# Performance work log

Hardware: AMD Instinct MI355X
Metric: run time of the kernel (lower is better)

The kernel has to match this reference:

```python
import jax, jax.numpy as jnp
import numpy as np

N = 524288
NUM_LEVELS = 16
FEATS = 2
LOG2_T = 19
TABLE = 1 << LOG2_T
MIN_RES, MAX_RES = 16, 1024
PRIMES = np.array([1, 2654435761, 805459861], dtype=np.uint32)
_growth = np.exp((np.log(MAX_RES) - np.log(MIN_RES)) / (NUM_LEVELS - 1))
SCALINGS = np.floor(MIN_RES * _growth ** np.arange(NUM_LEVELS)).astype(np.float32)  # [L]


def hash_encode(positions, table):
    # positions [N,3] in [0,1]; table [L*T, F]
    scaled = positions[:, None, :] * jnp.asarray(SCALINGS)[None, :, None]  # [N,L,3]
    fl = jnp.floor(scaled)
    ce = jnp.ceil(scaled)
    offset = scaled - fl  # [N,L,3]
    primes = jnp.asarray(PRIMES)  # [3] uint32
    lvl_off = jnp.arange(NUM_LEVELS, dtype=jnp.uint32) * jnp.uint32(TABLE)  # [L]
    out = jnp.zeros(scaled.shape[:2] + (FEATS,), scaled.dtype)
    for corner in range(8):
        bits = np.array([(corner >> d) & 1 for d in range(3)], dtype=np.float32)
        coord = jnp.where(jnp.asarray(bits, dtype=bool), ce, fl)
        h = coord.astype(jnp.int32).astype(jnp.uint32) * primes  # [N,L,3]
        h = h[..., 0] ^ h[..., 1] ^ h[..., 2]
        idx = ((h & jnp.uint32(TABLE - 1)) + lvl_off).astype(jnp.int32)  # [N,L]
        b = jnp.asarray(bits)
        w = jnp.prod(b * offset + (1.0 - b) * (1.0 - offset), axis=-1, keepdims=True)  # [N,L,1]
        out = out + w * table[idx]
    return out.reshape(out.shape[0], NUM_LEVELS * FEATS)  # [N,32]


def nerf_encode(d):
    # NeRFEncoding: 4 freqs in 2**linspace(0,4,4), include_input=True -> 27 dims
    freqs = 2.0 ** jnp.linspace(0.0, 4.0, 4)
    scaled = (2.0 * jnp.pi * d)[..., None] * freqs  # [N,3,4]
    scaled = scaled.reshape(d.shape[0], -1)  # [N,12]
    enc = jnp.sin(jnp.concatenate([scaled, scaled + jnp.pi / 2.0], axis=-1))  # [N,24]
    return jnp.concatenate([enc, d], axis=-1)  # [N,27]


def setup_inputs() -> dict:
    key = jax.random.key(0)
    ks = jax.random.split(key, 16)
    w = lambda k, i, o: jax.random.normal(k, (i, o), jnp.float32) * (1.0 / np.sqrt(i))
    return {
        "positions": jax.random.uniform(ks[0], (N, 3), jnp.float32),
        "directions": jax.random.normal(ks[1], (N, 3), jnp.float32),
        "hash_table": (jax.random.uniform(ks[2], (NUM_LEVELS * TABLE, FEATS), jnp.float32) * 2.0 - 1.0) * 1e-3,
        "w0": w(ks[3], 32, 64), "b0": jnp.zeros((64,), jnp.float32),
        "w1": w(ks[4], 64, 64), "b1": jnp.zeros((64,), jnp.float32),
        "w2": w(ks[5], 64, 64), "b2": jnp.zeros((64,), jnp.float32),
        "wr": w(ks[6], 91, 32), "br": jnp.zeros((32,), jnp.float32),
        "wc": w(ks[7], 32, 3), "bc": jnp.zeros((3,), jnp.float32),
        "wd": w(ks[8], 64, 1), "bd": jnp.zeros((1,), jnp.float32),
    }


def reference(positions, directions, hash_table, w0, b0, w1, b1, w2, b2, wr, br, wc, bc, wd, bd):
    enc_xyz = hash_encode(positions, hash_table)  # [N,32]
    enc_dir = nerf_encode(directions)  # [N,27]
    h = jax.nn.relu(enc_xyz @ w0 + b0)
    h = jax.nn.relu(h @ w1 + b1)
    base = h @ w2 + b2  # [N,64], linear out (out_activation=None)
    rgb_h = jnp.concatenate([enc_dir, base], axis=-1) @ wr + br  # [N,32], single layer
    rgb = jax.nn.sigmoid(rgb_h @ wc + bc)  # [N,3]
    density = jax.nn.softplus(base @ wd + bd)  # [N,1]
    return jnp.concatenate([rgb, density], axis=-1)  # [N,4]
```

## Files before the change

kernel.cpp:

```cpp
#include <hip/hip_runtime.h>
#include <math.h>

#define NPTS 524288
#define LOG2T 19
#define TSIZE (1u << LOG2T)
#define TMASK (TSIZE - 1u)

typedef unsigned int uint32;
typedef unsigned short ushort16;

typedef __attribute__((ext_vector_type(8))) short short8;
typedef __attribute__((ext_vector_type(4))) float f32x4;

__device__ __forceinline__ float bf2f(ushort16 u) {
    union { uint32 i; float f; } v; v.i = ((uint32)u) << 16; return v.f;
}
__device__ __forceinline__ ushort16 f2bf(float f) {
    union { float f; uint32 i; } v; v.f = f;
    uint32 r = v.i + 0x7fffu + ((v.i >> 16) & 1u);
    return (ushort16)(r >> 16);
}
__device__ __forceinline__ uint32 pack2(float a, float b) {
    uint32 r;
    asm("v_cvt_pk_bf16_f32 %0, %1, %2" : "=v"(r) : "v"(a), "v"(b));
    return r;
}
__device__ __forceinline__ float ldin(const void* p, int i, bool f32) {
    return f32 ? ((const float*)p)[i] : bf2f(((const ushort16*)p)[i]);
}

struct Scal16 { float s[16]; };
struct Freq4  { float f[4]; };
struct HashP  { float s[16]; int dD[8]; int doff[8]; };
struct DenseP { int dD[6]; int pfx[7]; };

__global__ __launch_bounds__(256) void k_prep(const void* __restrict__ pos,
                                              const void* __restrict__ tbl,
                                              uint4* __restrict__ tbl2F,
                                              uint4* __restrict__ dense4,
                                              DenseP dp) {
    __shared__ int sFlag;
    int tid = threadIdx.x;
    if (tid < 64) {
        const ushort16* ph = (const ushort16*)pos;
        float v0 = bf2f(ph[tid]), v1 = bf2f(ph[tid + 64]);
        bool odd = !(fabsf(v0) <= 4.f) || !(fabsf(v1) <= 4.f);
        unsigned long long m = __ballot(odd);
        if (tid == 0) sFlag = (m != 0ull) ? 1 : 0;
    }
    __syncthreads();
    const bool f32 = (sFlag != 0);

    if (blockIdx.x < 5120) {
        if (!f32) return;
        const float4* tf4 = (const float4*)tbl;
        size_t g = (size_t)blockIdx.x * 256 + tid;
        float4 v0 = tf4[(size_t)3 * TSIZE + 2 * g];
        float4 v1 = tf4[(size_t)3 * TSIZE + 2 * g + 1];
        uint4 o;
        o.x = pack2(v0.x, v0.y); o.y = pack2(v0.z, v0.w);
        o.z = pack2(v1.x, v1.y); o.w = pack2(v1.z, v1.w);
        tbl2F[g] = o;
        return;
    }

    int e = (blockIdx.x - 5120) * 256 + tid;
    if (e >= dp.pfx[6]) return;
    int l = 0;
#pragma unroll
    for (int k = 1; k < 6; ++k) l += (e >= dp.pfx[k]) ? 1 : 0;
    int c = e - dp.pfx[l];
    int D = dp.dD[l], D2 = D * D;
    int cz = c / D2; int rm = c - cz * D2;
    int cy = rm / D; int cx = rm - cy * D;

    uint32 base = (uint32)l << LOG2T;
    uint32 hz  = (uint32)cz * 805459861u;
    uint32 hy0 = (uint32)cy * 2654435761u;
    uint32 hy1 = (uint32)(cy + 1) * 2654435761u;
    uint32 h00 = ((((uint32)cx)       ^ hy0 ^ hz) & TMASK) + base;
    uint32 h10 = ((((uint32)(cx + 1)) ^ hy0 ^ hz) & TMASK) + base;
    uint32 h01 = ((((uint32)cx)       ^ hy1 ^ hz) & TMASK) + base;
    uint32 h11 = ((((uint32)(cx + 1)) ^ hy1 ^ hz) & TMASK) + base;

    uint4 o;
    if (f32) {
        const float2* t2 = (const float2*)tbl;
        float2 a = t2[h00], b = t2[h10], cc = t2[h01], d = t2[h11];
        o.x = pack2(a.x, a.y); o.y = pack2(b.x, b.y);
        o.z = pack2(cc.x, cc.y); o.w = pack2(d.x, d.y);
    } else {
        const uint32* t1 = (const uint32*)tbl;
        o.x = t1[h00]; o.y = t1[h10]; o.z = t1[h01]; o.w = t1[h11];
    }
    dense4[e] = o;
}

__global__ __launch_bounds__(256) void k_denseEnc(const void* __restrict__ pos,
                                                  const uint4* __restrict__ dense4,
                                                  uint32* __restrict__ enc,
                                                  HashP hp) {
    __shared__ __align__(16) uint4 sPosQ[192];
    __shared__ int sFlag;
    int tid = threadIdx.x;
    if (tid < 64) {
        const ushort16* ph = (const ushort16*)pos;
        float v0 = bf2f(ph[tid]), v1 = bf2f(ph[tid + 64]);
        bool odd = !(fabsf(v0) <= 4.f) || !(fabsf(v1) <= 4.f);
        unsigned long long m = __ballot(odd);
        if (tid == 0) sFlag = (m != 0ull) ? 1 : 0;
    }
    __syncthreads();
    const bool f32 = (sFlag != 0);

    int p0 = blockIdx.x * 256;
    int pt = p0 + tid;

    {
        int n16 = f32 ? 192 : 96;
        const uint4* src = (const uint4*)((const char*)pos + (size_t)p0 * (f32 ? 12 : 6));
        for (int i = tid; i < n16; i += 256) sPosQ[i] = src[i];
    }
    __syncthreads();

    float x, y, z;
    if (f32) {
        const float* pf = (const float*)sPosQ;
        x = pf[3 * tid]; y = pf[3 * tid + 1]; z = pf[3 * tid + 2];
    } else {
        const ushort16* ph2 = (const ushort16*)sPosQ;
        x = bf2f(ph2[3 * tid]); y = bf2f(ph2[3 * tid + 1]); z = bf2f(ph2[3 * tid + 2]);
    }

#pragma unroll
    for (int l = 0; l < 6; ++l) {
        float s = hp.s[l];
        float sx = x * s, sy = y * s, sz = z * s;
        float fx = floorf(sx), fy = floorf(sy), fz = floorf(sz);
        float cx = ceilf(sx), cy = ceilf(sy), cz = ceilf(sz);
        float ox = sx - fx, oy = sy - fy, oz = sz - fz;
        float wx0 = 1.f - ox, wy0 = 1.f - oy, wz0 = 1.f - oz;

        int D = hp.dD[l], D2 = D * D;
        int fxi = (int)fx, fyi = (int)fy, fzi = (int)fz;
        bool dxb = ((int)cx != fxi);
        bool dyb = ((int)cy != fyi);
        bool dzb = ((int)cz != fzi);
        const uint4* dp4 = dense4 + hp.doff[l];
        int i0 = fxi + fyi * D + fzi * D2;
        uint4 P0 = dp4[i0];
        uint4 P1 = dp4[i0 + (dzb ? D2 : 0)];

        float a0 = 0.f, a1 = 0.f;
        {
            uint32 fv = P0.x, cv = dxb ? P0.y : P0.x;
            float w = wy0 * wz0;
            a0 += w * (wx0 * bf2f((ushort16)(fv & 0xffffu)) + ox * bf2f((ushort16)(cv & 0xffffu)));
            a1 += w * (wx0 * bf2f((ushort16)(fv >> 16))     + ox * bf2f((ushort16)(cv >> 16)));
        }
        {
            uint32 fv = dyb ? P0.z : P0.x;
            uint32 cv = dyb ? (dxb ? P0.w : P0.z) : (dxb ? P0.y : P0.x);
            float w = oy * wz0;
            a0 += w * (wx0 * bf2f((ushort16)(fv & 0xffffu)) + ox * bf2f((ushort16)(cv & 0xffffu)));
            a1 += w * (wx0 * bf2f((ushort16)(fv >> 16))     + ox * bf2f((ushort16)(cv >> 16)));
        }
        {
            uint32 fv = P1.x, cv = dxb ? P1.y : P1.x;
            float w = wy0 * oz;
            a0 += w * (wx0 * bf2f((ushort16)(fv & 0xffffu)) + ox * bf2f((ushort16)(cv & 0xffffu)));
            a1 += w * (wx0 * bf2f((ushort16)(fv >> 16))     + ox * bf2f((ushort16)(cv >> 16)));
        }
        {
            uint32 fv = dyb ? P1.z : P1.x;
            uint32 cv = dyb ? (dxb ? P1.w : P1.z) : (dxb ? P1.y : P1.x);
            float w = oy * oz;
            a0 += w * (wx0 * bf2f((ushort16)(fv & 0xffffu)) + ox * bf2f((ushort16)(cv & 0xffffu)));
            a1 += w * (wx0 * bf2f((ushort16)(fv >> 16))     + ox * bf2f((ushort16)(cv >> 16)));
        }
        enc[(size_t)l * NPTS + pt] = pack2(a0, a1);
    }
}

__global__ __launch_bounds__(256) void k_hashB(const void* __restrict__ pos,
                                               const void* __restrict__ tbl,
                                               const uint32* __restrict__ tbl2F,
                                               uint32* __restrict__ enc,
                                               HashP hp) {
    __shared__ __align__(16) uint4 sPosQ[192];
    __shared__ int sFlag;
    int tid = threadIdx.x;
    if (tid < 64) {
        const ushort16* ph = (const ushort16*)pos;
        float v0 = bf2f(ph[tid]), v1 = bf2f(ph[tid + 64]);
        bool odd = !(fabsf(v0) <= 4.f) || !(fabsf(v1) <= 4.f);
        unsigned long long m = __ballot(odd);
        if (tid == 0) sFlag = (m != 0ull) ? 1 : 0;
    }
    __syncthreads();
    const bool f32 = (sFlag != 0);

    int xcd = blockIdx.x & 7;
    int slot = blockIdx.x >> 3;
    int W = xcd * 2560 + slot;
    int lvl = 6 + (W >> 11);
    int chunk = W & 2047;
    int p0 = chunk * 256;
    int pt = p0 + tid;

    {
        int n16 = f32 ? 192 : 96;
        const uint4* src = (const uint4*)((const char*)pos + (size_t)p0 * (f32 ? 12 : 6));
        for (int i = tid; i < n16; i += 256) sPosQ[i] = src[i];
    }
    __syncthreads();

    float x, y, z;
    if (f32) {
        const float* pf = (const float*)sPosQ;
        x = pf[3 * tid]; y = pf[3 * tid + 1]; z = pf[3 * tid + 2];
    } else {
        const ushort16* ph2 = (const ushort16*)sPosQ;
        x = bf2f(ph2[3 * tid]); y = bf2f(ph2[3 * tid + 1]); z = bf2f(ph2[3 * tid + 2]);
    }

    float s = hp.s[lvl];
    float sx = x * s, sy = y * s, sz = z * s;
    float fx = floorf(sx), fy = floorf(sy), fz = floorf(sz);
    float cx = ceilf(sx), cy = ceilf(sy), cz = ceilf(sz);
    float ox = sx - fx, oy = sy - fy, oz = sz - fz;
    float wx0 = 1.f - ox, wy0 = 1.f - oy, wz0 = 1.f - oz;

    const uint32* tp; uint32 base;
    if (f32) { tp = tbl2F; base = (uint32)(lvl - 6) << LOG2T; }
    else     { tp = (const uint32*)tbl; base = (uint32)lvl << LOG2T; }
    uint32 hx0 = (uint32)(int)fx;
    uint32 hx1 = (uint32)(int)cx;
    uint32 hy0 = (uint32)(int)fy * 2654435761u;
    uint32 hy1 = (uint32)(int)cy * 2654435761u;
    uint32 hz0 = (uint32)(int)fz * 805459861u;
    uint32 hz1 = (uint32)(int)cz * 805459861u;

    float a0 = 0.f, a1 = 0.f;
#pragma unroll
    for (int yz = 0; yz < 4; ++yz) {
        uint32 m = ((yz & 1) ? hy1 : hy0) ^ ((yz & 2) ? hz1 : hz0);
        float wyz = ((yz & 1) ? oy : wy0) * ((yz & 2) ? oz : wz0);
        uint32 i0 = ((hx0 ^ m) & TMASK) + base;
        uint32 i1 = ((hx1 ^ m) & TMASK) + base;
        uint32 d0, d1;
        if (i1 == (i0 ^ 1u)) {
            uint2 pv = *(const uint2*)(tp + (i0 & ~1u));
            d0 = (i0 & 1u) ? pv.y : pv.x;
            d1 = (i0 & 1u) ? pv.x : pv.y;
        } else {
            d0 = tp[i0]; d1 = tp[i1];
        }
        a0 += wyz * (wx0 * bf2f((ushort16)(d0 & 0xffffu)) + ox * bf2f((ushort16)(d1 & 0xffffu)));
        a1 += wyz * (wx0 * bf2f((ushort16)(d0 >> 16))     + ox * bf2f((ushort16)(d1 >> 16)));
    }
    enc[(size_t)lvl * NPTS + pt] = pack2(a0, a1);
}

__global__ __launch_bounds__(256) void k_hash(const void* __restrict__ pos,
                                              const void* __restrict__ tbl,
                                              uint32* __restrict__ enc,
                                              Scal16 sc) {
    __shared__ int sFlag;
    int tid = threadIdx.x;
    if (tid < 64) {
        const ushort16* ph = (const ushort16*)pos;
        float v0 = bf2f(ph[tid]), v1 = bf2f(ph[tid + 64]);
        bool odd = !(fabsf(v0) <= 4.f) || !(fabsf(v1) <= 4.f);
        unsigned long long m = __ballot(odd);
        if (tid == 0) sFlag = (m != 0ull) ? 1 : 0;
    }
    __syncthreads();
    const bool f32 = (sFlag != 0);

    int lvl = ((blockIdx.x >> 14) << 3) + (blockIdx.x & 7);
    int pt = ((blockIdx.x >> 3) & 2047) * 256 + tid;

    float s = sc.s[lvl];
    float x = ldin(pos, 3 * pt, f32), y = ldin(pos, 3 * pt + 1, f32), z = ldin(pos, 3 * pt + 2, f32);
    float sx = x * s, sy = y * s, sz = z * s;
    float fx = floorf(sx), fy = floorf(sy), fz = floorf(sz);
    float cx = ceilf(sx), cy = ceilf(sy), cz = ceilf(sz);
    float ox = sx - fx, oy = sy - fy, oz = sz - fz;
    uint32 hx0 = (uint32)(int)fx;
    uint32 hx1 = (uint32)(int)cx;
    uint32 hy0 = (uint32)(int)fy * 2654435761u;
    uint32 hy1 = (uint32)(int)cy * 2654435761u;
    uint32 hz0 = (uint32)(int)fz * 805459861u;
    uint32 hz1 = (uint32)(int)cz * 805459861u;
    uint32 base = (uint32)lvl << LOG2T;
    float wx0 = 1.f - ox, wy0 = 1.f - oy, wz0 = 1.f - oz;

    float a0 = 0.f, a1 = 0.f;
    if (f32) {
        const float* tf = (const float*)tbl;
#pragma unroll
        for (int yz = 0; yz < 4; ++yz) {
            uint32 m = ((yz & 1) ? hy1 : hy0) ^ ((yz & 2) ? hz1 : hz0);
            float wyz = ((yz & 1) ? oy : wy0) * ((yz & 2) ? oz : wz0);
            uint32 i0 = ((hx0 ^ m) & TMASK) + base;
            uint32 i1 = ((hx1 ^ m) & TMASK) + base;
            float4 pv = *(const float4*)(tf + (size_t)(i0 & ~1u) * 2);
            bool lo = !(i0 & 1u);
            float f0 = lo ? pv.x : pv.z, f1 = lo ? pv.y : pv.w;
            float c0, c1;
            if (i1 == (i0 ^ 1u)) { c0 = lo ? pv.z : pv.x; c1 = lo ? pv.w : pv.y; }
            else { float2 tv = ((const float2*)tbl)[i1]; c0 = tv.x; c1 = tv.y; }
            a0 += wyz * (wx0 * f0 + ox * c0);
            a1 += wyz * (wx0 * f1 + ox * c1);
        }
    } else {
#pragma unroll
        for (int cr = 0; cr < 8; ++cr) {
            uint32 h = ((cr & 1) ? hx1 : hx0) ^ ((cr & 2) ? hy1 : hy0) ^ ((cr & 4) ? hz1 : hz0);
            uint32 idx = (h & TMASK) + base;
            uint32 dv = ((const uint32*)tbl)[idx];
            float w = ((cr & 1) ? ox : wx0) * ((cr & 2) ? oy : wy0) * ((cr & 4) ? oz : wz0);
            a0 += w * bf2f((ushort16)(dv & 0xffffu));
            a1 += w * bf2f((ushort16)(dv >> 16));
        }
    }
    enc[(size_t)lvl * NPTS + pt] = pack2(a0, a1);
}

#define STRY 76
#define STRW0 40
#define STRW12 76
#define STRWR 104
#define MSTRX 100
#define PPI 128
#define NIT (NPTS / PPI)

__global__ __launch_bounds__(512) void k_mlp(
    const void* __restrict__ pos,
    const uint32* __restrict__ enc, const void* __restrict__ dirs,
    const void* __restrict__ w0, const void* __restrict__ b0,
    const void* __restrict__ w1, const void* __restrict__ b1,
    const void* __restrict__ w2, const void* __restrict__ b2,
    const void* __restrict__ wr, const void* __restrict__ br,
    const void* __restrict__ wc, const void* __restrict__ bc,
    const void* __restrict__ wd, const void* __restrict__ bd,
    void* __restrict__ out, Freq4 fq)
{
    __shared__ __align__(16) ushort16 sX[PPI * MSTRX];
    __shared__ __align__(16) ushort16 sY[PPI * STRY];
    __shared__ __align__(16) ushort16 sW0[64 * STRW0];
    __shared__ __align__(16) ushort16 sW1[64 * STRW12];
    __shared__ __align__(16) ushort16 sW2[64 * STRW12];
    __shared__ __align__(16) ushort16 sWR[32 * STRWR];
    __shared__ __align__(16) ushort16 sW4[16 * STRWR];
    __shared__ __align__(16) float sB0[64], sB1[64], sB2[64], sBR[32], sFB[4];
    __shared__ int sFlag;

    int tid = threadIdx.x;

    if (tid < 64) {
        const ushort16* ph = (const ushort16*)pos;
        float v0 = bf2f(ph[tid]), v1 = bf2f(ph[tid + 64]);
        bool odd = !(fabsf(v0) <= 4.f) || !(fabsf(v1) <= 4.f);
        unsigned long long m = __ballot(odd);
        if (tid == 0) sFlag = (m != 0ull) ? 1 : 0;
    }
    __syncthreads();
    const bool f32 = (sFlag != 0);

    for (int i = tid; i < 2048; i += 512) { int k = i >> 6, n = i & 63; sW0[n * STRW0 + k] = f2bf(ldin(w0, i, f32)); }
    for (int i = tid; i < 4096; i += 512) { int k = i >> 6, n = i & 63; sW1[n * STRW12 + k] = f2bf(ldin(w1, i, f32)); }
    for (int i = tid; i < 4096; i += 512) { int k = i >> 6, n = i & 63; sW2[n * STRW12 + k] = f2bf(ldin(w2, i, f32)); }
    for (int i = tid; i < 2912; i += 512) {
        int r = i >> 5, n = i & 31; int k = (r < 27) ? r : r + 5;
        sWR[n * STRWR + k] = f2bf(ldin(wr, i, f32));
    }
    if (tid < 160) { int n = tid / 5, k = 27 + tid % 5; sWR[n * STRWR + k] = 0; }
    for (int i = tid; i < 1536; i += 512) {
        int n = i / 96, j = i % 96;
        float v = 0.f;
        if (n == 3 && j < 64) v = ldin(wd, j, f32);
        else if (n < 3 && j >= 64) v = ldin(wc, (j - 64) * 3 + n, f32);
        sW4[n * STRWR + j] = f2bf(v);
    }
    if (tid < 64) { sB0[tid] = ldin(b0, tid, f32); sB1[tid] = ldin(b1, tid, f32); sB2[tid] = ldin(b2, tid, f32); }
    if (tid < 32) sBR[tid] = ldin(br, tid, f32);
    if (tid < 3) sFB[tid] = ldin(bc, tid, f32);
    if (tid == 3) sFB[3] = ldin(bd, 0, f32);

    int lane = tid & 63, wv = tid >> 6;
    int colg = lane & 15, quad = lane >> 4;
    int myrow = wv * 16 + colg;

    for (int c = blockIdx.x; c < NIT; c += gridDim.x) {
        int p0 = c * PPI;
        __syncthreads();

        for (int i = tid; i < 1024; i += 512) {
            int l = i & 15, pp = (i >> 4) * 2;
            uint2 e = *(const uint2*)&enc[(size_t)l * NPTS + p0 + pp];
            *(uint32*)&sX[pp * MSTRX + 2 * l] = e.x;
            *(uint32*)&sX[(pp + 1) * MSTRX + 2 * l] = e.y;
        }
        if (tid < 384) {
            int p = tid / 3, i2 = tid - 3 * (tid / 3);
            float dvv = ldin(dirs, 3 * (p0 + p) + i2, f32);
            ushort16* row = &sX[p * MSTRX + 64];
            float td = 6.28318530717958647692f * dvv;
            float a0 = td * fq.f[0], a1 = td * fq.f[1], a2 = td * fq.f[2], a3 = td * fq.f[3];
            uint2 sv, cv;
            sv.x = pack2(__sinf(a0), __sinf(a1));
            sv.y = pack2(__sinf(a2), __sinf(a3));
            cv.x = pack2(__cosf(a0), __cosf(a1));
            cv.y = pack2(__cosf(a2), __cosf(a3));
            *(uint2*)&row[i2 * 4] = sv;
            *(uint2*)&row[12 + i2 * 4] = cv;
            row[24 + i2] = f2bf(dvv);
        } else {
            int p = tid - 384;
            ushort16* row = &sX[p * MSTRX + 64];
#pragma unroll
            for (int j = 27; j < 32; ++j) row[j] = 0;
        }
        __syncthreads();

        {
            short8 xb = *(const short8*)&sX[myrow * MSTRX + quad * 8];
#pragma unroll
            for (int nt = 0; nt < 4; ++nt) {
                short8 a = *(const short8*)&sW0[(nt * 16 + colg) * STRW0 + quad * 8];
                f32x4 acc = {0.f, 0.f, 0.f, 0.f};
                acc = __builtin_amdgcn_mfma_f32_16x16x32_bf16(a, xb, acc, 0, 0, 0);
                float4 bi = *(const float4*)&sB0[nt * 16 + quad * 4];
                uint2 o;
                o.x = pack2(fmaxf(acc[0] + bi.x, 0.f), fmaxf(acc[1] + bi.y, 0.f));
                o.y = pack2(fmaxf(acc[2] + bi.z, 0.f), fmaxf(acc[3] + bi.w, 0.f));
                *(uint2*)&sY[myrow * STRY + nt * 16 + quad * 4] = o;
            }
        }
        {
            short8 xb0 = *(const short8*)&sY[myrow * STRY + quad * 8];
            short8 xb1 = *(const short8*)&sY[myrow * STRY + 32 + quad * 8];
#pragma unroll
            for (int nt = 0; nt < 4; ++nt) {
                short8 a0 = *(const short8*)&sW1[(nt * 16 + colg) * STRW12 + quad * 8];
                short8 a1 = *(const short8*)&sW1[(nt * 16 + colg) * STRW12 + 32 + quad * 8];
                f32x4 acc = {0.f, 0.f, 0.f, 0.f};
                acc = __builtin_amdgcn_mfma_f32_16x16x32_bf16(a0, xb0, acc, 0, 0, 0);
                acc = __builtin_amdgcn_mfma_f32_16x16x32_bf16(a1, xb1, acc, 0, 0, 0);
                float4 bi = *(const float4*)&sB1[nt * 16 + quad * 4];
                uint2 o;
                o.x = pack2(fmaxf(acc[0] + bi.x, 0.f), fmaxf(acc[1] + bi.y, 0.f));
                o.y = pack2(fmaxf(acc[2] + bi.z, 0.f), fmaxf(acc[3] + bi.w, 0.f));
                *(uint2*)&sX[myrow * MSTRX + nt * 16 + quad * 4] = o;
            }
        }
        {
            short8 xb0 = *(const short8*)&sX[myrow * MSTRX + quad * 8];
            short8 xb1 = *(const short8*)&sX[myrow * MSTRX + 32 + quad * 8];
#pragma unroll
            for (int nt = 0; nt < 4; ++nt) {
                short8 a0 = *(const short8*)&sW2[(nt * 16 + colg) * STRW12 + quad * 8];
                short8 a1 = *(const short8*)&sW2[(nt * 16 + colg) * STRW12 + 32 + quad * 8];
                f32x4 acc = {0.f, 0.f, 0.f, 0.f};
                acc = __builtin_amdgcn_mfma_f32_16x16x32_bf16(a0, xb0, acc, 0, 0, 0);
                acc = __builtin_amdgcn_mfma_f32_16x16x32_bf16(a1, xb1, acc, 0, 0, 0);
                float4 bi = *(const float4*)&sB2[nt * 16 + quad * 4];
                uint2 o;
                o.x = pack2(acc[0] + bi.x, acc[1] + bi.y);
                o.y = pack2(acc[2] + bi.z, acc[3] + bi.w);
                *(uint2*)&sY[myrow * STRY + nt * 16 + quad * 4] = o;
            }
        }
        {
            short8 xb0 = *(const short8*)&sX[myrow * MSTRX + 64 + quad * 8];
            short8 xb1 = *(const short8*)&sY[myrow * STRY + quad * 8];
            short8 xb2 = *(const short8*)&sY[myrow * STRY + 32 + quad * 8];
#pragma unroll
            for (int nt = 0; nt < 2; ++nt) {
                short8 a0 = *(const short8*)&sWR[(nt * 16 + colg) * STRWR + quad * 8];
                short8 a1 = *(const short8*)&sWR[(nt * 16 + colg) * STRWR + 32 + quad * 8];
                short8 a2 = *(const short8*)&sWR[(nt * 16 + colg) * STRWR + 64 + quad * 8];
                f32x4 acc = {0.f, 0.f, 0.f, 0.f};
                acc = __builtin_amdgcn_mfma_f32_16x16x32_bf16(a0, xb0, acc, 0, 0, 0);
                acc = __builtin_amdgcn_mfma_f32_16x16x32_bf16(a1, xb1, acc, 0, 0, 0);
                acc = __builtin_amdgcn_mfma_f32_16x16x32_bf16(a2, xb2, acc, 0, 0, 0);
                float4 bi = *(const float4*)&sBR[nt * 16 + quad * 4];
                uint2 o;
                o.x = pack2(acc[0] + bi.x, acc[1] + bi.y);
                o.y = pack2(acc[2] + bi.z, acc[3] + bi.w);
                *(uint2*)&sX[myrow * MSTRX + nt * 16 + quad * 4] = o;
            }
        }
        {
            short8 xb0 = *(const short8*)&sY[myrow * STRY + quad * 8];
            short8 xb1 = *(const short8*)&sY[myrow * STRY + 32 + quad * 8];
            short8 xb2 = *(const short8*)&sX[myrow * MSTRX + quad * 8];
            short8 a0 = *(const short8*)&sW4[colg * STRWR + quad * 8];
            short8 a1 = *(const short8*)&sW4[colg * STRWR + 32 + quad * 8];
            short8 a2 = *(const short8*)&sW4[colg * STRWR + 64 + quad * 8];
            f32x4 acc = {0.f, 0.f, 0.f, 0.f};
            acc = __builtin_amdgcn_mfma_f32_16x16x32_bf16(a0, xb0, acc, 0, 0, 0);
            acc = __builtin_amdgcn_mfma_f32_16x16x32_bf16(a1, xb1, acc, 0, 0, 0);
            acc = __builtin_amdgcn_mfma_f32_16x16x32_bf16(a2, xb2, acc, 0, 0, 0);
            if (quad == 0) {
                float r0 = acc[0] + sFB[0], r1 = acc[1] + sFB[1], r2 = acc[2] + sFB[2], dd = acc[3] + sFB[3];
                r0 = 1.f / (1.f + expf(-r0));
                r1 = 1.f / (1.f + expf(-r1));
                r2 = 1.f / (1.f + expf(-r2));
                float sp = (dd > 0.f) ? (dd + log1pf(expf(-dd))) : log1pf(expf(dd));
                int pt = p0 + myrow;
                if (f32) {
                    float4 o4; o4.x = r0; o4.y = r1; o4.z = r2; o4.w = sp;
                    ((float4*)out)[pt] = o4;
                } else {
                    uint2 o; o.x = pack2(r0, r1); o.y = pack2(r2, sp);
                    ((uint2*)out)[pt] = o;
                }
            }
        }
    }
}

#define FSTRX 104
__global__ __launch_bounds__(256) void k_fused(
    const void* __restrict__ pos, const void* __restrict__ dirs,
    const void* __restrict__ tbl,
    const void* __restrict__ w0, const void* __restrict__ b0,
    const void* __restrict__ w1, const void* __restrict__ b1,
    const void* __restrict__ w2, const void* __restrict__ b2,
    const void* __restrict__ wr, const void* __restrict__ br,
    const void* __restrict__ wc, const void* __restrict__ bc,
    const void* __restrict__ wd, const void* __restrict__ bd,
    void* __restrict__ out, Scal16 sc, Freq4 fq)
{
    __shared__ __align__(16) ushort16 sX[64 * FSTRX];
    __shared__ __align__(16) ushort16 sY[64 * STRY];
    __shared__ __align__(16) ushort16 sW0[64 * STRW0];
    __shared__ __align__(16) ushort16 sW1[64 * STRW12];
    __shared__ __align__(16) ushort16 sW2[64 * STRW12];
    __shared__ __align__(16) ushort16 sWR[32 * STRWR];
    __shared__ float sB0[64], sB1[64], sB2[64], sBR[32];
    __shared__ float sWCf[100];
    __shared__ float sWDf[64];
    __shared__ float sPosF[192];
    __shared__ int sFlag;

    int tid = threadIdx.x;
    if (tid < 64) {
        const ushort16* ph = (const ushort16*)pos;
        float v0 = bf2f(ph[tid]), v1 = bf2f(ph[tid + 64]);
        bool odd = !(fabsf(v0) <= 4.f) || !(fabsf(v1) <= 4.f);
        unsigned long long m = __ballot(odd);
        if (tid == 0) sFlag = (m != 0ull) ? 1 : 0;
    }
    __syncthreads();
    const bool f32 = (sFlag != 0);

    for (int i = tid; i < 2048; i += 256) { int k = i >> 6, n = i & 63; sW0[n * STRW0 + k] = f2bf(ldin(w0, i, f32)); }
    for (int i = tid; i < 4096; i += 256) { int k = i >> 6, n = i & 63; sW1[n * STRW12 + k] = f2bf(ldin(w1, i, f32)); }
    for (int i = tid; i < 4096; i += 256) { int k = i >> 6, n = i & 63; sW2[n * STRW12 + k] = f2bf(ldin(w2, i, f32)); }
    for (int i = tid; i < 2912; i += 256) {
        int r = i >> 5, n = i & 31; int k = (r < 27) ? r : r + 5;
        sWR[n * STRWR + k] = f2bf(ldin(wr, i, f32));
    }
    if (tid < 160) { int n = tid / 5, k = 27 + tid % 5; sWR[n * STRWR + k] = 0; }
    if (tid < 64) { sB0[tid] = ldin(b0, tid, f32); sB1[tid] = ldin(b1, tid, f32);
                    sB2[tid] = ldin(b2, tid, f32); sWDf[tid] = ldin(wd, tid, f32); }
    if (tid < 32) sBR[tid] = ldin(br, tid, f32);
    if (tid < 96) sWCf[tid] = ldin(wc, tid, f32);
    if (tid == 96) { sWCf[96] = ldin(bc, 0, f32); sWCf[97] = ldin(bc, 1, f32);
                     sWCf[98] = ldin(bc, 2, f32); sWCf[99] = ldin(bd, 0, f32); }

    int lane = tid & 63, wv = tid >> 6;
    int colg = lane & 15, quad = lane >> 4;
    int myl = tid & 15;
    float mys = sc.s[myl];
    uint32 mybase = (uint32)myl << LOG2T;

    for (int c = blockIdx.x; c < NPTS / 64; c += gridDim.x) {
        int p0 = c * 64;
        __syncthreads();
        if (tid < 192) sPosF[tid] = ldin(pos, p0 * 3 + tid, f32);
        __syncthreads();
#pragma unroll
        for (int ii = 0; ii < 4; ++ii) {
            int p = (tid >> 4) + 16 * ii;
            float x = sPosF[3 * p], y = sPosF[3 * p + 1], z = sPosF[3 * p + 2];
            float sx = x * mys, sy = y * mys, sz = z * mys;
            float fx = floorf(sx), fy = floorf(sy), fz = floorf(sz);
            float cx = ceilf(sx), cy = ceilf(sy), cz = ceilf(sz);
            float ox = sx - fx, oy = sy - fy, oz = sz - fz;
            uint32 hx0 = (uint32)(int)fx;
            uint32 hx1 = (uint32)(int)cx;
            uint32 hy0 = (uint32)(int)fy * 2654435761u;
            uint32 hy1 = (uint32)(int)cy * 2654435761u;
            uint32 hz0 = (uint32)(int)fz * 805459861u;
            uint32 hz1 = (uint32)(int)cz * 805459861u;
            float wx0 = 1.f - ox, wy0 = 1.f - oy, wz0 = 1.f - oz;
            float a0 = 0.f, a1 = 0.f;
#pragma unroll
            for (int cr = 0; cr < 8; ++cr) {
                uint32 h = ((cr & 1) ? hx1 : hx0) ^ ((cr & 2) ? hy1 : hy0) ^ ((cr & 4) ? hz1 : hz0);
                uint32 idx = (h & TMASK) + mybase;
                float t0, t1;
                if (f32) { float2 tv = ((const float2*)tbl)[idx]; t0 = tv.x; t1 = tv.y; }
                else { uint32 dv = ((const uint32*)tbl)[idx]; t0 = bf2f((ushort16)(dv & 0xffffu)); t1 = bf2f((ushort16)(dv >> 16)); }
                float w = ((cr & 1) ? ox : wx0) * ((cr & 2) ? oy : wy0) * ((cr & 4) ? oz : wz0);
                a0 += w * t0; a1 += w * t1;
            }
            *(uint32*)&sX[p * FSTRX + 2 * myl] = pack2(a0, a1);
        }
        __syncthreads();
        {
            short8 a = *(const short8*)&sX[(wv * 16 + colg) * FSTRX + quad * 8];
#pragma unroll
            for (int nt = 0; nt < 4; ++nt) {
                short8 bb = *(const short8*)&sW0[(nt * 16 + colg) * STRW0 + quad * 8];
                f32x4 acc = {0.f, 0.f, 0.f, 0.f};
                acc = __builtin_amdgcn_mfma_f32_16x16x32_bf16(a, bb, acc, 0, 0, 0);
                float bias = sB0[nt * 16 + colg];
#pragma unroll
                for (int r = 0; r < 4; ++r) {
                    float v = fmaxf(acc[r] + bias, 0.f);
                    sY[(wv * 16 + quad * 4 + r) * STRY + nt * 16 + colg] = f2bf(v);
                }
            }
        }
        __syncthreads();
        {
            short8 a0 = *(const short8*)&sY[(wv * 16 + colg) * STRY + quad * 8];
            short8 a1 = *(const short8*)&sY[(wv * 16 + colg) * STRY + 32 + quad * 8];
#pragma unroll
            for (int nt = 0; nt < 4; ++nt) {
                short8 bb0 = *(const short8*)&sW1[(nt * 16 + colg) * STRW12 + quad * 8];
                short8 bb1 = *(const short8*)&sW1[(nt * 16 + colg) * STRW12 + 32 + quad * 8];
                f32x4 acc = {0.f, 0.f, 0.f, 0.f};
                acc = __builtin_amdgcn_mfma_f32_16x16x32_bf16(a0, bb0, acc, 0, 0, 0);
                acc = __builtin_amdgcn_mfma_f32_16x16x32_bf16(a1, bb1, acc, 0, 0, 0);
                float bias = sB1[nt * 16 + colg];
#pragma unroll
                for (int r = 0; r < 4; ++r) {
                    float v = fmaxf(acc[r] + bias, 0.f);
                    sX[(wv * 16 + quad * 4 + r) * FSTRX + nt * 16 + colg] = f2bf(v);
                }
            }
        }
        __syncthreads();
        {
            short8 a0 = *(const short8*)&sX[(wv * 16 + colg) * FSTRX + quad * 8];
            short8 a1 = *(const short8*)&sX[(wv * 16 + colg) * FSTRX + 32 + quad * 8];
#pragma unroll
            for (int nt = 0; nt < 4; ++nt) {
                short8 bb0 = *(const short8*)&sW2[(nt * 16 + colg) * STRW12 + quad * 8];
                short8 bb1 = *(const short8*)&sW2[(nt * 16 + colg) * STRW12 + 32 + quad * 8];
                f32x4 acc = {0.f, 0.f, 0.f, 0.f};
                acc = __builtin_amdgcn_mfma_f32_16x16x32_bf16(a0, bb0, acc, 0, 0, 0);
                acc = __builtin_amdgcn_mfma_f32_16x16x32_bf16(a1, bb1, acc, 0, 0, 0);
                float bias = sB2[nt * 16 + colg];
#pragma unroll
                for (int r = 0; r < 4; ++r) {
                    sY[(wv * 16 + quad * 4 + r) * STRY + nt * 16 + colg] = f2bf(acc[r] + bias);
                }
            }
        }
        if (tid < 192) {
            int p = tid / 3, i2 = tid % 3;
            float dvv = ldin(dirs, 3 * (p0 + p) + i2, f32);
            ushort16* row = &sX[p * FSTRX + 64];
            float td = 6.28318530717958647692f * dvv;
#pragma unroll
            for (int j = 0; j < 4; ++j) {
                float arg = td * fq.f[j];
                float sv, cv;
                sincosf(arg, &sv, &cv);
                row[i2 * 4 + j] = f2bf(sv);
                row[12 + i2 * 4 + j] = f2bf(cv);
            }
            row[24 + i2] = f2bf(dvv);
        } else {
            int p = tid - 192;
            ushort16* row = &sX[p * FSTRX + 64];
#pragma unroll
            for (int j = 27; j < 32; ++j) row[j] = 0;
        }
        __syncthreads();
        {
            short8 a0 = *(const short8*)&sX[(wv * 16 + colg) * FSTRX + 64 + quad * 8];
            short8 a1 = *(const short8*)&sY[(wv * 16 + colg) * STRY + quad * 8];
            short8 a2 = *(const short8*)&sY[(wv * 16 + colg) * STRY + 32 + quad * 8];
#pragma unroll
            for (int nt = 0; nt < 2; ++nt) {
                short8 bb0 = *(const short8*)&sWR[(nt * 16 + colg) * STRWR + quad * 8];
                short8 bb1 = *(const short8*)&sWR[(nt * 16 + colg) * STRWR + 32 + quad * 8];
                short8 bb2 = *(const short8*)&sWR[(nt * 16 + colg) * STRWR + 64 + quad * 8];
                f32x4 acc = {0.f, 0.f, 0.f, 0.f};
                acc = __builtin_amdgcn_mfma_f32_16x16x32_bf16(a0, bb0, acc, 0, 0, 0);
                acc = __builtin_amdgcn_mfma_f32_16x16x32_bf16(a1, bb1, acc, 0, 0, 0);
                acc = __builtin_amdgcn_mfma_f32_16x16x32_bf16(a2, bb2, acc, 0, 0, 0);
                float bias = sBR[nt * 16 + colg];
#pragma unroll
                for (int r = 0; r < 4; ++r) {
                    sX[(wv * 16 + quad * 4 + r) * FSTRX + nt * 16 + colg] = f2bf(acc[r] + bias);
                }
            }
        }
        __syncthreads();
        if (tid < 64) {
            int pt = p0 + tid;
            float r0 = 0.f, r1 = 0.f, r2 = 0.f, dd = 0.f;
            const ushort16* hx = &sX[tid * FSTRX];
            const ushort16* hb = &sY[tid * STRY];
#pragma unroll
            for (int k = 0; k < 32; ++k) {
                float hv = bf2f(hx[k]);
                r0 += hv * sWCf[k * 3 + 0];
                r1 += hv * sWCf[k * 3 + 1];
                r2 += hv * sWCf[k * 3 + 2];
            }
#pragma unroll
            for (int k = 0; k < 64; ++k) dd += bf2f(hb[k]) * sWDf[k];
            r0 += sWCf[96]; r1 += sWCf[97]; r2 += sWCf[98]; dd += sWCf[99];
            r0 = 1.f / (1.f + expf(-r0));
            r1 = 1.f / (1.f + expf(-r1));
            r2 = 1.f / (1.f + expf(-r2));
            float sp = (dd > 0.f) ? (dd + log1pf(expf(-dd))) : log1pf(expf(dd));
            if (f32) {
                float4 o4; o4.x = r0; o4.y = r1; o4.z = r2; o4.w = sp;
                ((float4*)out)[pt] = o4;
            } else {
                uint2 o;
                o.x = pack2(r0, r1); o.y = pack2(r2, sp);
                ((uint2*)out)[pt] = o;
            }
        }
    }
}

extern "C" void kernel_launch(void* const* d_in, const int* in_sizes, int n_in,
                              void* d_out, int out_size, void* d_ws, size_t ws_size,
                              hipStream_t stream) {
    (void)in_sizes; (void)n_in; (void)out_size;

    Scal16 sc;
    double g = exp((log(1024.0) - log(16.0)) / 15.0);
    for (int l = 0; l < 16; ++l) sc.s[l] = (float)floor(16.0 * pow(g, (double)l));

    Freq4 fq;
    float lv[4] = {0.f, 4.f / 3.f, 8.f / 3.f, 4.f};
    for (int j = 0; j < 4; ++j) fq.f[j] = (float)pow(2.0, (double)lv[j]);

    DenseP dpp;
    HashP hp;
    dpp.pfx[0] = 0;
    for (int l = 0; l < 6; ++l) {
        int D = (int)sc.s[l] + 1;
        dpp.dD[l] = D;
        dpp.pfx[l + 1] = dpp.pfx[l] + D * D * D;
    }
    for (int l = 0; l < 16; ++l) hp.s[l] = sc.s[l];
    for (int l = 0; l < 8; ++l) {
        hp.dD[l]   = (l < 6) ? dpp.dD[l] : 1;
        hp.doff[l] = (l < 6) ? dpp.pfx[l] : 0;
    }
    int ndense = dpp.pfx[6];

    const size_t enc_bytes   = (size_t)16 * NPTS * 4;
    const size_t tbl2F_bytes = (size_t)10 * TSIZE * 4;
    const size_t dense_bytes = (size_t)ndense * 16 + 64;
    const size_t need_new = enc_bytes + tbl2F_bytes + dense_bytes;

    if (ws_size >= need_new) {
        uint32* enc   = (uint32*)d_ws;
        uint32* tbl2F = (uint32*)((char*)d_ws + enc_bytes);
        uint4*  dense4 = (uint4*)((char*)d_ws + enc_bytes + tbl2F_bytes);
        int nprep = 5120 + (ndense + 255) / 256;
        k_prep<<<dim3(nprep), dim3(256), 0, stream>>>(d_in[0], d_in[2], (uint4*)tbl2F, dense4, dpp);
        k_denseEnc<<<dim3(NPTS / 256), dim3(256), 0, stream>>>(d_in[0], dense4, enc, hp);
        k_hashB<<<dim3(10 * NPTS / 256), dim3(256), 0, stream>>>(d_in[0], d_in[2], tbl2F, enc, hp);
        k_mlp<<<dim3(512), dim3(512), 0, stream>>>(
            d_in[0], enc, d_in[1], d_in[3], d_in[4], d_in[5], d_in[6], d_in[7],
            d_in[8], d_in[9], d_in[10], d_in[11], d_in[12], d_in[13], d_in[14],
            d_out, fq);
    } else if (ws_size >= enc_bytes) {
        uint32* enc = (uint32*)d_ws;
        k_hash<<<dim3(2 * 8 * NPTS / 256), dim3(256), 0, stream>>>(d_in[0], d_in[2], enc, sc);
        k_mlp<<<dim3(512), dim3(512), 0, stream>>>(
            d_in[0], enc, d_in[1], d_in[3], d_in[4], d_in[5], d_in[6], d_in[7],
            d_in[8], d_in[9], d_in[10], d_in[11], d_in[12], d_in[13], d_in[14],
            d_out, fq);
    } else {
        k_fused<<<dim3(512), dim3(256), 0, stream>>>(
            d_in[0], d_in[1], d_in[2], d_in[3], d_in[4], d_in[5], d_in[6], d_in[7],
            d_in[8], d_in[9], d_in[10], d_in[11], d_in[12], d_in[13], d_in[14],
            d_out, sc, fq);
    }
}
```

Measured before the change: 315.8 us.

## Fuse dense-level hash interpolation into MLP kernel, drop k_denseEnc launch

Removes the separate k_denseEnc kernel and computes the six dense-grid levels directly inside k_mlp. In each tile, 128 threads interpolate those levels from dense4 while the other 384 threads compute the direction encoding and load the remaining ten hashed levels from enc. This saves one kernel launch and the write and re-read of six encoding planes in global memory. In exchange, the interpolation now sits on the MLP kernel's critical path, with only a quarter of its threads doing the gathers, which could add latency and imbalance inside each tile.

```diff
diff --git a/kernel.cpp b/kernel.cpp
--- a/kernel.cpp
+++ b/kernel.cpp
@@ -33,6 +33,55 @@
 struct Freq4  { float f[4]; };
 struct HashP  { float s[16]; int dD[8]; int doff[8]; };
 struct DenseP { int dD[6]; int pfx[7]; };
+
+__device__ __forceinline__ uint32 dense_interp(const uint4* __restrict__ dense4,
+                                               float x, float y, float z,
+                                               float s, int D, int doff) {
+    float sx = x * s, sy = y * s, sz = z * s;
+    float fx = floorf(sx), fy = floorf(sy), fz = floorf(sz);
+    float cx = ceilf(sx), cy = ceilf(sy), cz = ceilf(sz);
+    float ox = sx - fx, oy = sy - fy, oz = sz - fz;
+    float wx0 = 1.f - ox, wy0 = 1.f - oy, wz0 = 1.f - oz;
+
+    int D2 = D * D;
+    int fxi = (int)fx, fyi = (int)fy, fzi = (int)fz;
+    bool dxb = ((int)cx != fxi);
+    bool dyb = ((int)cy != fyi);
+    bool dzb = ((int)cz != fzi);
+    const uint4* dp4 = dense4 + doff;
+    int i0 = fxi + fyi * D + fzi * D2;
+    uint4 P0 = dp4[i0];
+    uint4 P1 = dp4[i0 + (dzb ? D2 : 0)];
+
+    float a0 = 0.f, a1 = 0.f;
+    {
+        uint32 fv = P0.x, cv = dxb ? P0.y : P0.x;
+        float w = wy0 * wz0;
+        a0 += w * (wx0 * bf2f((ushort16)(fv & 0xffffu)) + ox * bf2f((ushort16)(cv & 0xffffu)));
+        a1 += w * (wx0 * bf2f((ushort16)(fv >> 16))     + ox * bf2f((ushort16)(cv >> 16)));
+    }
+    {
+        uint32 fv = dyb ? P0.z : P0.x;
+        uint32 cv = dyb ? (dxb ? P0.w : P0.z) : (dxb ? P0.y : P0.x);
+        float w = oy * wz0;
+        a0 += w * (wx0 * bf2f((ushort16)(fv & 0xffffu)) + ox * bf2f((ushort16)(cv & 0xffffu)));
+        a1 += w * (wx0 * bf2f((ushort16)(fv >> 16))     + ox * bf2f((ushort16)(cv >> 16)));
+    }
+    {
+        uint32 fv = P1.x, cv = dxb ? P1.y : P1.x;
+        float w = wy0 * oz;
+        a0 += w * (wx0 * bf2f((ushort16)(fv & 0xffffu)) + ox * bf2f((ushort16)(cv & 0xffffu)));
+        a1 += w * (wx0 * bf2f((ushort16)(fv >> 16))     + ox * bf2f((ushort16)(cv >> 16)));
+    }
+    {
+        uint32 fv = dyb ? P1.z : P1.x;
+        uint32 cv = dyb ? (dxb ? P1.w : P1.z) : (dxb ? P1.y : P1.x);
+        float w = oy * oz;
+        a0 += w * (wx0 * bf2f((ushort16)(fv & 0xffffu)) + ox * bf2f((ushort16)(cv & 0xffffu)));
+        a1 += w * (wx0 * bf2f((ushort16)(fv >> 16))     + ox * bf2f((ushort16)(cv >> 16)));
+    }
+    return pack2(a0, a1);
+}
 
 __global__ __launch_bounds__(256) void k_prep(const void* __restrict__ pos,
                                               const void* __restrict__ tbl,
@@ -94,92 +143,6 @@
         o.x = t1[h00]; o.y = t1[h10]; o.z = t1[h01]; o.w = t1[h11];
     }
     dense4[e] = o;
-}
-
-__global__ __launch_bounds__(256) void k_denseEnc(const void* __restrict__ pos,
-                                                  const uint4* __restrict__ dense4,
-                                                  uint32* __restrict__ enc,
-                                                  HashP hp) {
-    __shared__ __align__(16) uint4 sPosQ[192];
-    __shared__ int sFlag;
-    int tid = threadIdx.x;
-    if (tid < 64) {
-        const ushort16* ph = (const ushort16*)pos;
-        float v0 = bf2f(ph[tid]), v1 = bf2f(ph[tid + 64]);
-        bool odd = !(fabsf(v0) <= 4.f) || !(fabsf(v1) <= 4.f);
-        unsigned long long m = __ballot(odd);
-        if (tid == 0) sFlag = (m != 0ull) ? 1 : 0;
-    }
-    __syncthreads();
-    const bool f32 = (sFlag != 0);
-
-    int p0 = blockIdx.x * 256;
-    int pt = p0 + tid;
-
-    {
-        int n16 = f32 ? 192 : 96;
-        const uint4* src = (const uint4*)((const char*)pos + (size_t)p0 * (f32 ? 12 : 6));
-        for (int i = tid; i < n16; i += 256) sPosQ[i] = src[i];
-    }
-    __syncthreads();
-
-    float x, y, z;
-    if (f32) {
-        const float* pf = (const float*)sPosQ;
-        x = pf[3 * tid]; y = pf[3 * tid + 1]; z = pf[3 * tid + 2];
-    } else {
-        const ushort16* ph2 = (const ushort16*)sPosQ;
-        x = bf2f(ph2[3 * tid]); y = bf2f(ph2[3 * tid + 1]); z = bf2f(ph2[3 * tid + 2]);
-    }
-
-#pragma unroll
-    for (int l = 0; l < 6; ++l) {
-        float s = hp.s[l];
-        float sx = x * s, sy = y * s, sz = z * s;
-        float fx = floorf(sx), fy = floorf(sy), fz = floorf(sz);
-        float cx = ceilf(sx), cy = ceilf(sy), cz = ceilf(sz);
-        float ox = sx - fx, oy = sy - fy, oz = sz - fz;
-        float wx0 = 1.f - ox, wy0 = 1.f - oy, wz0 = 1.f - oz;
-
-        int D = hp.dD[l], D2 = D * D;
-        int fxi = (int)fx, fyi = (int)fy, fzi = (int)fz;
-        bool dxb = ((int)cx != fxi);
-        bool dyb = ((int)cy != fyi);
-        bool dzb = ((int)cz != fzi);
-        const uint4* dp4 = dense4 + hp.doff[l];
-        int i0 = fxi + fyi * D + fzi * D2;
-        uint4 P0 = dp4[i0];
-        uint4 P1 = dp4[i0 + (dzb ? D2 : 0)];
-
-        float a0 = 0.f, a1 = 0.f;
-        {
-            uint32 fv = P0.x, cv = dxb ? P0.y : P0.x;
-            float w = wy0 * wz0;
-            a0 += w * (wx0 * bf2f((ushort16)(fv & 0xffffu)) + ox * bf2f((ushort16)(cv & 0xffffu)));
-            a1 += w * (wx0 * bf2f((ushort16)(fv >> 16))     + ox * bf2f((ushort16)(cv >> 16)));
-        }
-        {
-            uint32 fv = dyb ? P0.z : P0.x;
-            uint32 cv = dyb ? (dxb ? P0.w : P0.z) : (dxb ? P0.y : P0.x);
-            float w = oy * wz0;
-            a0 += w * (wx0 * bf2f((ushort16)(fv & 0xffffu)) + ox * bf2f((ushort16)(cv & 0xffffu)));
-            a1 += w * (wx0 * bf2f((ushort16)(fv >> 16))     + ox * bf2f((ushort16)(cv >> 16)));
-        }
-        {
-            uint32 fv = P1.x, cv = dxb ? P1.y : P1.x;
-            float w = wy0 * oz;
-            a0 += w * (wx0 * bf2f((ushort16)(fv & 0xffffu)) + ox * bf2f((ushort16)(cv & 0xffffu)));
-            a1 += w * (wx0 * bf2f((ushort16)(fv >> 16))     + ox * bf2f((ushort16)(cv >> 16)));
-        }
-        {
-            uint32 fv = dyb ? P1.z : P1.x;
-            uint32 cv = dyb ? (dxb ? P1.w : P1.z) : (dxb ? P1.y : P1.x);
-            float w = oy * oz;
-            a0 += w * (wx0 * bf2f((ushort16)(fv & 0xffffu)) + ox * bf2f((ushort16)(cv & 0xffffu)));
-            a1 += w * (wx0 * bf2f((ushort16)(fv >> 16))     + ox * bf2f((ushort16)(cv >> 16)));
-        }
-        enc[(size_t)l * NPTS + pt] = pack2(a0, a1);
-    }
 }
 
 __global__ __launch_bounds__(256) void k_hashB(const void* __restrict__ pos,
@@ -339,13 +302,14 @@
 __global__ __launch_bounds__(512) void k_mlp(
     const void* __restrict__ pos,
     const uint32* __restrict__ enc, const void* __restrict__ dirs,
+    const uint4* __restrict__ dense4,
     const void* __restrict__ w0, const void* __restrict__ b0,
     const void* __restrict__ w1, const void* __restrict__ b1,
     const void* __restrict__ w2, const void* __restrict__ b2,
     const void* __restrict__ wr, const void* __restrict__ br,
     const void* __restrict__ wc, const void* __restrict__ bc,
     const void* __restrict__ wd, const void* __restrict__ bd,
-    void* __restrict__ out, Freq4 fq)
+    void* __restrict__ out, Freq4 fq, HashP hp, int denseMode)
 {
     __shared__ __align__(16) ushort16 sX[PPI * MSTRX];
     __shared__ __align__(16) ushort16 sY[PPI * STRY];
@@ -397,31 +361,75 @@
         int p0 = c * PPI;
         __syncthreads();
 
-        for (int i = tid; i < 1024; i += 512) {
-            int l = i & 15, pp = (i >> 4) * 2;
-            uint2 e = *(const uint2*)&enc[(size_t)l * NPTS + p0 + pp];
-            *(uint32*)&sX[pp * MSTRX + 2 * l] = e.x;
-            *(uint32*)&sX[(pp + 1) * MSTRX + 2 * l] = e.y;
-        }
-        if (tid < 384) {
-            int p = tid / 3, i2 = tid - 3 * (tid / 3);
-            float dvv = ldin(dirs, 3 * (p0 + p) + i2, f32);
-            ushort16* row = &sX[p * MSTRX + 64];
-            float td = 6.28318530717958647692f * dvv;
-            float a0 = td * fq.f[0], a1 = td * fq.f[1], a2 = td * fq.f[2], a3 = td * fq.f[3];
-            uint2 sv, cv;
-            sv.x = pack2(__sinf(a0), __sinf(a1));
-            sv.y = pack2(__sinf(a2), __sinf(a3));
-            cv.x = pack2(__cosf(a0), __cosf(a1));
-            cv.y = pack2(__cosf(a2), __cosf(a3));
-            *(uint2*)&row[i2 * 4] = sv;
-            *(uint2*)&row[12 + i2 * 4] = cv;
-            row[24 + i2] = f2bf(dvv);
+        if (denseMode) {
+            if (tid < 128) {
+                int pt = p0 + tid;
+                float x, y, z;
+                if (f32) {
+                    const float* pf = (const float*)pos;
+                    x = pf[3 * pt]; y = pf[3 * pt + 1]; z = pf[3 * pt + 2];
+                } else {
+                    const ushort16* ph2 = (const ushort16*)pos;
+                    x = bf2f(ph2[3 * pt]); y = bf2f(ph2[3 * pt + 1]); z = bf2f(ph2[3 * pt + 2]);
+                }
+                ushort16* row = &sX[tid * MSTRX];
+#pragma unroll
+                for (int l = 0; l < 6; ++l) {
+                    *(uint32*)&row[2 * l] = dense_interp(dense4, x, y, z, hp.s[l], hp.dD[l], hp.doff[l]);
+                }
+#pragma unroll
+                for (int j = 27; j < 32; ++j) row[64 + j] = 0;
+            } else {
+                int t = tid - 128;
+                {
+                    int p = t / 3, i2 = t - 3 * (t / 3);
+                    float dvv = ldin(dirs, 3 * (p0 + p) + i2, f32);
+                    ushort16* row = &sX[p * MSTRX + 64];
+                    float td = 6.28318530717958647692f * dvv;
+                    float a0 = td * fq.f[0], a1 = td * fq.f[1], a2 = td * fq.f[2], a3 = td * fq.f[3];
+                    uint2 sv, cv;
+                    sv.x = pack2(__sinf(a0), __sinf(a1));
+                    sv.y = pack2(__sinf(a2), __sinf(a3));
+                    cv.x = pack2(__cosf(a0), __cosf(a1));
+                    cv.y = pack2(__cosf(a2), __cosf(a3));
+                    *(uint2*)&row[i2 * 4] = sv;
+                    *(uint2*)&row[12 + i2 * 4] = cv;
+                    row[24 + i2] = f2bf(dvv);
+                }
+                for (int i = t; i < 640; i += 384) {
+                    int l = i % 10; int pp = (i / 10) * 2;
+                    uint2 e = *(const uint2*)&enc[(size_t)(6 + l) * NPTS + p0 + pp];
+                    *(uint32*)&sX[pp * MSTRX + 12 + 2 * l] = e.x;
+                    *(uint32*)&sX[(pp + 1) * MSTRX + 12 + 2 * l] = e.y;
+                }
+            }
         } else {
-            int p = tid - 384;
-            ushort16* row = &sX[p * MSTRX + 64];
-#pragma unroll
-            for (int j = 27; j < 32; ++j) row[j] = 0;
+            for (int i = tid; i < 1024; i += 512) {
+                int l = i & 15, pp = (i >> 4) * 2;
+                uint2 e = *(const uint2*)&enc[(size_t)l * NPTS + p0 + pp];
+                *(uint32*)&sX[pp * MSTRX + 2 * l] = e.x;
+                *(uint32*)&sX[(pp + 1) * MSTRX + 2 * l] = e.y;
+            }
+            if (tid < 384) {
+                int p = tid / 3, i2 = tid - 3 * (tid / 3);
+                float dvv = ldin(dirs, 3 * (p0 + p) + i2, f32);
+                ushort16* row = &sX[p * MSTRX + 64];
+                float td = 6.28318530717958647692f * dvv;
+                float a0 = td * fq.f[0], a1 = td * fq.f[1], a2 = td * fq.f[2], a3 = td * fq.f[3];
+                uint2 sv, cv;
+                sv.x = pack2(__sinf(a0), __sinf(a1));
+                sv.y = pack2(__sinf(a2), __sinf(a3));
+                cv.x = pack2(__cosf(a0), __cosf(a1));
+                cv.y = pack2(__cosf(a2), __cosf(a3));
+                *(uint2*)&row[i2 * 4] = sv;
+                *(uint2*)&row[12 + i2 * 4] = cv;
+                row[24 + i2] = f2bf(dvv);
+            } else {
+                int p = tid - 384;
+                ushort16* row = &sX[p * MSTRX + 64];
+#pragma unroll
+                for (int j = 27; j < 32; ++j) row[j] = 0;
+            }
         }
         __syncthreads();
 
@@ -777,19 +785,18 @@
         uint4*  dense4 = (uint4*)((char*)d_ws + enc_bytes + tbl2F_bytes);
         int nprep = 5120 + (ndense + 255) / 256;
         k_prep<<<dim3(nprep), dim3(256), 0, stream>>>(d_in[0], d_in[2], (uint4*)tbl2F, dense4, dpp);
-        k_denseEnc<<<dim3(NPTS / 256), dim3(256), 0, stream>>>(d_in[0], dense4, enc, hp);
         k_hashB<<<dim3(10 * NPTS / 256), dim3(256), 0, stream>>>(d_in[0], d_in[2], tbl2F, enc, hp);
         k_mlp<<<dim3(512), dim3(512), 0, stream>>>(
-            d_in[0], enc, d_in[1], d_in[3], d_in[4], d_in[5], d_in[6], d_in[7],
+            d_in[0], enc, d_in[1], dense4, d_in[3], d_in[4], d_in[5], d_in[6], d_in[7],
             d_in[8], d_in[9], d_in[10], d_in[11], d_in[12], d_in[13], d_in[14],
-            d_out, fq);
+            d_out, fq, hp, 1);
     } else if (ws_size >= enc_bytes) {
         uint32* enc = (uint32*)d_ws;
         k_hash<<<dim3(2 * 8 * NPTS / 256), dim3(256), 0, stream>>>(d_in[0], d_in[2], enc, sc);
         k_mlp<<<dim3(512), dim3(512), 0, stream>>>(
-            d_in[0], enc, d_in[1], d_in[3], d_in[4], d_in[5], d_in[6], d_in[7],
+            d_in[0], enc, d_in[1], (const uint4*)d_ws , d_in[3], d_in[4], d_in[5], d_in[6], d_in[7],
             d_in[8], d_in[9], d_in[10], d_in[11], d_in[12], d_in[13], d_in[14],
-            d_out, fq);
+            d_out, fq, hp, 0);
     } else {
         k_fused<<<dim3(512), dim3(256), 0, stream>>>(
             d_in[0], d_in[1], d_in[2], d_in[3], d_in[4], d_in[5], d_in[6], d_in[7],
```

After: 296.1 us, median of 2. 6.2% less time.
